# Kernel tuning notes

Hardware: AMD Instinct MI355X
Metric: run time of the kernel (lower is better)

The kernel has to match this reference:

```python
import jax, jax.numpy as jnp
import numpy as np

N_SAMPLES, N_CHANNELS, LOOKBACK, N_ASSETS = 16, 64, 128, 64
HIDDEN = 512
HD = HIDDEN // 2  # per-direction hidden size (bidirectional)


def setup_inputs() -> dict:
    key = jax.random.key(0)
    ks = jax.random.split(key, 9)
    s = 1.0 / np.sqrt(HD)  # PyTorch LSTM init scale
    def u(k, shape):
        return jax.random.uniform(k, shape, jnp.float32, -s, s)
    return {
        "x": jax.random.normal(ks[0], (N_SAMPLES, N_CHANNELS, LOOKBACK, N_ASSETS), jnp.float32),
        "W_ih_f": u(ks[1], (4 * HD, N_CHANNELS)),
        "W_hh_f": u(ks[2], (4 * HD, HD)),
        "b_ih_f": u(ks[3], (4 * HD,)),
        "b_hh_f": u(ks[4], (4 * HD,)),
        "W_ih_b": u(ks[5], (4 * HD, N_CHANNELS)),
        "W_hh_b": u(ks[6], (4 * HD, HD)),
        "b_ih_b": u(ks[7], (4 * HD,)),
        "b_hh_b": u(ks[8], (4 * HD,)),
    }


def _lstm_dir(xp, W_hh, reverse):
    # xp: (T, B, 4*HD) precomputed input projections + biases
    B = xp.shape[1]
    h0 = jnp.zeros((B, HD), xp.dtype)
    c0 = jnp.zeros((B, HD), xp.dtype)

    def step(carry, g_x):
        h, c = carry
        g = g_x + h @ W_hh.T  # (B, 4*HD)
        i, f, gg, o = jnp.split(g, 4, axis=-1)  # PyTorch gate order i,f,g,o
        i = jax.nn.sigmoid(i)
        f = jax.nn.sigmoid(f)
        gg = jnp.tanh(gg)
        o = jax.nn.sigmoid(o)
        c = f * c + i * gg
        h = o * jnp.tanh(c)
        return (h, c), h

    _, hs = jax.lax.scan(step, (h0, c0), xp, reverse=reverse)
    return hs  # (T, B, HD), time-aligned (reverse scan keeps original order)


def reference(x, W_ih_f, W_hh_f, b_ih_f, b_hh_f, W_ih_b, W_hh_b, b_ih_b, b_hh_b):
    S, C, T, A = x.shape
    # (S, C, T, A) -> (T, S*A, C): fuse all samples+assets into one batch
    xs = jnp.transpose(x, (2, 0, 3, 1)).reshape(T, S * A, C)
    xp_f = jnp.einsum('tbc,gc->tbg', xs, W_ih_f) + b_ih_f + b_hh_f
    xp_b = jnp.einsum('tbc,gc->tbg', xs, W_ih_b) + b_ih_b + b_hh_b
    h_f = _lstm_dir(xp_f, W_hh_f, reverse=False)  # (T, S*A, HD)
    h_b = _lstm_dir(xp_b, W_hh_b, reverse=True)   # (T, S*A, HD)
    h = jnp.concatenate([h_f, h_b], axis=-1)      # (T, S*A, HIDDEN)
    # -> (S, HIDDEN, T, A)
    return jnp.transpose(h.reshape(T, S, A, HIDDEN), (1, 3, 0, 2))
```

## Files before the change

kernel.cpp:

```cpp
#include <hip/hip_runtime.h>

#define T_LEN 128
#define WF_OFF 0
#define BI_OFF 1310720
#define XZ_OFF 1441792
#define HZ_OFF 18219008
#define FL_OFF 20316160
#define WS_END 20332544

typedef short bf16x8 __attribute__((ext_vector_type(8)));
typedef float f32x4 __attribute__((ext_vector_type(4)));

#define WAITV0 asm volatile("s_waitcnt vmcnt(0)" ::: "memory")
#define SCHB __builtin_amdgcn_sched_barrier(0)

__device__ __forceinline__ short f32_to_bf16(float f) {
  unsigned u = __float_as_uint(f);
  unsigned r = u + 0x7FFFu + ((u >> 16) & 1u);
  return (short)(r >> 16);
}
__device__ __forceinline__ float sigmoidf_fast(float x) {
  return 1.0f / (1.0f + __expf(-x));
}
__device__ __forceinline__ float tanhf_fast(float x) {
  return 1.0f - 2.0f / (__expf(2.0f * x) + 1.0f);
}

__device__ __forceinline__ void gll16(const void* g, char* lds_generic) {
  __builtin_amdgcn_global_load_lds(
      (const __attribute__((address_space(1))) void*)g,
      (__attribute__((address_space(3))) void*)lds_generic, 16, 0, 0);
}
__device__ __forceinline__ bf16x8 ald16(const void* p) {
  bf16x8 d;
  asm volatile("global_load_dwordx4 %0, %1, off" : "=v"(d) : "v"(p));
  return d;
}
__device__ __forceinline__ f32x4 aldf4(const void* p) {
  f32x4 d;
  asm volatile("global_load_dwordx4 %0, %1, off" : "=v"(d) : "v"(p));
  return d;
}
__device__ __forceinline__ bf16x8 ald16_dev(const void* p) {
  bf16x8 d;
  asm volatile("global_load_dwordx4 %0, %1, off sc0 sc1" : "=v"(d) : "v"(p));
  return d;
}
__device__ __forceinline__ void ast16_dev(void* p, bf16x8 v) {
  asm volatile("global_store_dwordx4 %0, %1, off sc0 sc1" :: "v"(p), "v"(v));
}

__global__ void pack_w(const float* __restrict__ Wih_f, const float* __restrict__ Whh_f,
                       const float* __restrict__ Wih_b, const float* __restrict__ Whh_b,
                       short* __restrict__ wf) {
  int t = blockIdx.x * blockDim.x + threadIdx.x;
  int l = t & 63;
  int r1 = t >> 6;
  int kt = r1 % 10;
  int r2 = r1 / 10;
  int mtl = r2 & 7;
  int r3 = r2 >> 3;
  int m = r3 & 7;
  int dir = r3 >> 3;
  const float* Wih = dir ? Wih_b : Wih_f;
  const float* Whh = dir ? Whh_b : Whh_f;
  int rA = l & 15;
  int row = (rA & 3) * 256 + 32 * m + 4 * mtl + (rA >> 2);
  int kb = kt * 32 + (l >> 4) * 8;
  bf16x8 v;
#pragma unroll
  for (int e = 0; e < 8; ++e) {
    int k = kb + e;
    float f = (k < 64) ? Wih[row * 64 + k] : Whh[row * 256 + (k - 64)];
    v[e] = f32_to_bf16(f);
  }
  long idx = ((((long)dir * 8 + m) * 8 + mtl) * 10 + kt) * 64 + l;
  *reinterpret_cast<bf16x8*>(wf + idx * 8) = v;
}

__global__ void pack_bias(const float* __restrict__ bihf, const float* __restrict__ bhhf,
                          const float* __restrict__ bihb, const float* __restrict__ bhhb,
                          float* __restrict__ bp) {
  int t = blockIdx.x * blockDim.x + threadIdx.x;
  int l = t & 63;
  int mtl = (t >> 6) & 7;
  int m = (t >> 9) & 7;
  int dir = (t >> 12) & 1;
  const float* bih = dir ? bihb : bihf;
  const float* bhh = dir ? bhhb : bhhf;
  int u = 32 * m + 4 * mtl + ((l >> 4) & 3);
  f32x4 v;
#pragma unroll
  for (int r = 0; r < 4; ++r) v[r] = bih[r * 256 + u] + bhh[r * 256 + u];
  long idx = (((long)dir * 8 + m) * 8 + mtl) * 64 + l;
  *reinterpret_cast<f32x4*>(bp + idx * 4) = v;
}

__global__ void pack_x(const float* __restrict__ x, short* __restrict__ xz) {
  int t = blockIdx.x * blockDim.x + threadIdx.x;
  int cs = t & 7;
  int a  = (t >> 3) & 63;
  int tt = (t >> 9) & 127;
  int s  = (t >> 16) & 15;
  bf16x8 v;
#pragma unroll
  for (int e = 0; e < 8; ++e) {
    int c = cs * 8 + e;
    v[e] = f32_to_bf16(x[(((long)s * 64 + c) * 128 + tt) * 64 + a]);
  }
  long idx = (((long)s * 128 + tt) * 64 + a) * 64 + cs * 8;
  *reinterpret_cast<bf16x8*>(xz + idx) = v;
}

__global__ __launch_bounds__(512) void lstm_rec(
    const short* __restrict__ wf, const float* __restrict__ bp,
    const short* __restrict__ xz, short* __restrict__ hz,
    int* __restrict__ flags, float* __restrict__ out) {
  __shared__ __align__(16) char zbuf[40960];
  __shared__ __align__(16) char htr[4096];

  const int bid = blockIdx.x;
  const int m = bid >> 5, g = bid & 31;
  const int dir = g & 1, bb = g >> 1;
  const int tid = threadIdx.x;
  const int w = tid >> 6, l = tid & 63;
  const int lg = l >> 4, ln = l & 15;

  const char* wslice = (const char*)wf +
      ((((long)dir * 8 + m) * 8 + w) * 10) * 1024 + (long)l * 16;
  bf16x8 W0[10];
#pragma unroll
  for (int kt = 0; kt < 10; ++kt) W0[kt] = ald16(wslice + kt * 1024);
  const f32x4 bias4 = aldf4((const char*)bp +
      (((((long)dir * 8 + m) * 8 + w) * 64 + l) * 16));
  WAITV0;

  const char* xzb = (const char*)xz + (long)bb * (128L * 64 * 64 * 2);
  char* const hzg = (char*)hz + (long)g * (2L * 64 * 256 * 2);
  int* const flg = flags + g * T_LEN;

  float cst[4] = {0.f, 0.f, 0.f, 0.f};

  for (int st = 0; st < T_LEN; ++st) {
    const int t = dir ? (T_LEN - 1 - st) : st;

    if (st > 0 && tid == 0) {
      while (__hip_atomic_load(flg + (st - 1), __ATOMIC_RELAXED,
                               __HIP_MEMORY_SCOPE_AGENT) < 8)
        __builtin_amdgcn_s_sleep(2);
    }
    __syncthreads();

    {
      const char* xstep = xzb + (long)t * (64 * 64 * 2);
      {
        const int f = w, kt = f >> 2, nt = f & 3;
        gll16(xstep + (long)(((nt * 16 + ln) * 64 + kt * 32 + lg * 8) * 2),
              zbuf + f * 1024);
      }
      bf16x8 hstg[4];
      if (st == 0) {
#pragma unroll
        for (int j = 0; j < 4; ++j) hstg[j] = (bf16x8)(short)0;
      } else {
        const char* hprev = hzg + (long)((st + 1) & 1) * (64 * 256 * 2);
#pragma unroll
        for (int j = 0; j < 4; ++j) {
          const int f = 8 + 4 * w + j, kt = f >> 2, nt = f & 3;
          hstg[j] = ald16_dev(
              hprev + (long)(((nt * 16 + ln) * 256 + (kt - 2) * 32 + lg * 8) * 2));
        }
      }
      WAITV0; SCHB;
#pragma unroll
      for (int j = 0; j < 4; ++j)
        *reinterpret_cast<bf16x8*>(zbuf + (8 + 4 * w + j) * 1024 + l * 16) = hstg[j];
    }
    __syncthreads();

    f32x4 acc[4];
#pragma unroll
    for (int nt = 0; nt < 4; ++nt) acc[nt] = bias4;
#pragma unroll
    for (int kt = 0; kt < 10; ++kt)
#pragma unroll
      for (int nt = 0; nt < 4; ++nt) {
        bf16x8 b = *reinterpret_cast<const bf16x8*>(
            zbuf + (kt * 4 + nt) * 1024 + l * 16);
        acc[nt] = __builtin_amdgcn_mfma_f32_16x16x32_bf16(W0[kt], b, acc[nt], 0, 0, 0);
      }

    float hv[4];
#pragma unroll
    for (int nt = 0; nt < 4; ++nt) {
      float gi = sigmoidf_fast(acc[nt][0]);
      float gf = sigmoidf_fast(acc[nt][1]);
      float gg = tanhf_fast(acc[nt][2]);
      float go = sigmoidf_fast(acc[nt][3]);
      float cc = gf * cst[nt] + gi * gg;
      cst[nt] = cc;
      hv[nt] = go * tanhf_fast(cc);
    }
#pragma unroll
    for (int nt = 0; nt < 4; ++nt)
      *reinterpret_cast<short*>(htr + (nt * 16 + ln) * 64 + (4 * w + lg) * 2) =
          f32_to_bf16(hv[nt]);

    {
      const long hrow = (long)dir * 256 + 32 * m + 4 * w + lg;
#pragma unroll
      for (int nt = 0; nt < 4; ++nt) {
        const int a = nt * 16 + ln;
        out[(((long)bb * 512 + hrow) * 128 + t) * 64 + a] = hv[nt];
      }
    }
    __syncthreads();

    char* hcur = hzg + (long)(st & 1) * (64 * 256 * 2);
    if (tid < 256) {
      const int a = tid >> 2, seg = tid & 3;
      bf16x8 v = *reinterpret_cast<const bf16x8*>(htr + tid * 16);
      ast16_dev(hcur + (long)((a * 256 + 32 * m + seg * 8) * 2), v);
    }
    WAITV0;
    __syncthreads();
    if (tid == 0)
      __hip_atomic_fetch_add(flg + st, 1, __ATOMIC_RELAXED,
                             __HIP_MEMORY_SCOPE_AGENT);
  }
}

extern "C" void kernel_launch(void* const* d_in, const int* in_sizes, int n_in,
                              void* d_out, int out_size, void* d_ws, size_t ws_size,
                              hipStream_t stream) {
  const float* x     = (const float*)d_in[0];
  const float* Wih_f = (const float*)d_in[1];
  const float* Whh_f = (const float*)d_in[2];
  const float* bih_f = (const float*)d_in[3];
  const float* bhh_f = (const float*)d_in[4];
  const float* Wih_b = (const float*)d_in[5];
  const float* Whh_b = (const float*)d_in[6];
  const float* bih_b = (const float*)d_in[7];
  const float* bhh_b = (const float*)d_in[8];
  float* out = (float*)d_out;

  char* ws = (char*)d_ws;
  short* wf    = (short*)(ws + WF_OFF);
  float* bp    = (float*)(ws + BI_OFF);
  short* xz    = (short*)(ws + XZ_OFF);
  short* hz    = (short*)(ws + HZ_OFF);
  int*   flags = (int*)(ws + FL_OFF);

  hipLaunchKernelGGL(pack_w, dim3(320), dim3(256), 0, stream,
                     Wih_f, Whh_f, Wih_b, Whh_b, wf);
  hipLaunchKernelGGL(pack_bias, dim3(32), dim3(256), 0, stream,
                     bih_f, bhh_f, bih_b, bhh_b, bp);
  hipLaunchKernelGGL(pack_x, dim3(4096), dim3(256), 0, stream, x, xz);
  hipMemsetAsync(ws + FL_OFF, 0, WS_END - FL_OFF, stream);
  hipLaunchKernelGGL(lstm_rec, dim3(256), dim3(512), 0, stream,
                     wf, bp, xz, hz, flags, out);
}
```

Baseline: 627.4 us.

## Interleave forward and backward directions per block to hide inter-block sync latency

Each block now handles both LSTM directions for one sample and hidden slice, using 128 blocks instead of 256. It alternates forward and backward steps, so the cross-block flag wait and hidden-state exchange for one direction overlap with compute for the other. LDS buffers are doubled via dynamic shared memory, and the weights for both directions are held in registers. This halves parallelism and raises register and LDS pressure, in exchange for hiding the per-step global synchronization latency.

Measured after the change: 1.081 ms. +72.3%, slower.

```diff
diff --git a/kernel.cpp b/kernel.cpp
--- a/kernel.cpp
+++ b/kernel.cpp
@@ -7,6 +7,7 @@
 #define HZ_OFF 18219008
 #define FL_OFF 20316160
 #define WS_END 20332544
+#define SMEM_BYTES 90112
 
 typedef short bf16x8 __attribute__((ext_vector_type(8)));
 typedef float f32x4 __attribute__((ext_vector_type(4)));
@@ -116,118 +117,169 @@
     const short* __restrict__ wf, const float* __restrict__ bp,
     const short* __restrict__ xz, short* __restrict__ hz,
     int* __restrict__ flags, float* __restrict__ out) {
-  __shared__ __align__(16) char zbuf[40960];
-  __shared__ __align__(16) char htr[4096];
+  extern __shared__ char smem[];
+  char* const zbA = smem;
+  char* const zbB = smem + 40960;
+  char* const htA = smem + 81920;
+  char* const htB = smem + 86016;
 
   const int bid = blockIdx.x;
-  const int m = bid >> 5, g = bid & 31;
-  const int dir = g & 1, bb = g >> 1;
+  const int m = bid >> 4, s = bid & 15;
   const int tid = threadIdx.x;
   const int w = tid >> 6, l = tid & 63;
   const int lg = l >> 4, ln = l & 15;
 
-  const char* wslice = (const char*)wf +
-      ((((long)dir * 8 + m) * 8 + w) * 10) * 1024 + (long)l * 16;
-  bf16x8 W0[10];
-#pragma unroll
-  for (int kt = 0; kt < 10; ++kt) W0[kt] = ald16(wslice + kt * 1024);
-  const f32x4 bias4 = aldf4((const char*)bp +
-      (((((long)dir * 8 + m) * 8 + w) * 64 + l) * 16));
+  const char* wA = (const char*)wf + (((long)0 * 8 + m) * 8 + w) * 10 * 1024 + (long)l * 16;
+  const char* wB = (const char*)wf + (((long)1 * 8 + m) * 8 + w) * 10 * 1024 + (long)l * 16;
+  bf16x8 WA[10], WB[10];
+#pragma unroll
+  for (int kt = 0; kt < 10; ++kt) {
+    WA[kt] = ald16(wA + kt * 1024);
+    WB[kt] = ald16(wB + kt * 1024);
+  }
+  const f32x4 biasA = aldf4((const char*)bp +
+      ((((long)0 * 8 + m) * 8 + w) * 64 + l) * 16);
+  const f32x4 biasB = aldf4((const char*)bp +
+      ((((long)1 * 8 + m) * 8 + w) * 64 + l) * 16);
   WAITV0;
 
-  const char* xzb = (const char*)xz + (long)bb * (128L * 64 * 64 * 2);
-  char* const hzg = (char*)hz + (long)g * (2L * 64 * 256 * 2);
-  int* const flg = flags + g * T_LEN;
-
-  float cst[4] = {0.f, 0.f, 0.f, 0.f};
+  const char* xzb = (const char*)xz + (long)s * (128L * 64 * 64 * 2);
+  char* const hzA = (char*)hz + (long)(2 * s) * 65536;
+  char* const hzB = (char*)hz + (long)(2 * s + 1) * 65536;
+  int* const flgA = flags + (2 * s) * T_LEN;
+  int* const flgB = flags + (2 * s + 1) * T_LEN;
+
+  float cstA[4] = {0.f, 0.f, 0.f, 0.f};
+  float cstB[4] = {0.f, 0.f, 0.f, 0.f};
+
+  {
+    const char* xstep = xzb;
+    const int kt = w >> 2, nt = w & 3;
+    gll16(xstep + (long)(((nt * 16 + ln) * 64 + kt * 32 + lg * 8) * 2),
+          zbA + w * 1024);
+    bf16x8 z8 = (bf16x8)(short)0;
+#pragma unroll
+    for (int j = 0; j < 4; ++j)
+      *reinterpret_cast<bf16x8*>(zbA + (8 + 4 * w + j) * 1024 + l * 16) = z8;
+  }
+  WAITV0;
+  __syncthreads();
+
+#define COMPUTE(ZB, HT, W_, BIAS, CST, T_, DIRQ) do {                         \
+    f32x4 acc[4];                                                             \
+    _Pragma("unroll")                                                         \
+    for (int nt = 0; nt < 4; ++nt) acc[nt] = (BIAS);                          \
+    _Pragma("unroll")                                                         \
+    for (int kt = 0; kt < 10; ++kt)                                           \
+      _Pragma("unroll")                                                       \
+      for (int nt = 0; nt < 4; ++nt) {                                        \
+        bf16x8 b = *reinterpret_cast<const bf16x8*>(                          \
+            (ZB) + (kt * 4 + nt) * 1024 + l * 16);                            \
+        acc[nt] = __builtin_amdgcn_mfma_f32_16x16x32_bf16(W_[kt], b, acc[nt], 0, 0, 0); \
+      }                                                                       \
+    float hv[4];                                                              \
+    _Pragma("unroll")                                                         \
+    for (int nt = 0; nt < 4; ++nt) {                                          \
+      float gi = sigmoidf_fast(acc[nt][0]);                                   \
+      float gf = sigmoidf_fast(acc[nt][1]);                                   \
+      float gg = tanhf_fast(acc[nt][2]);                                      \
+      float go = sigmoidf_fast(acc[nt][3]);                                   \
+      float cc = gf * (CST)[nt] + gi * gg;                                    \
+      (CST)[nt] = cc;                                                         \
+      hv[nt] = go * tanhf_fast(cc);                                           \
+    }                                                                         \
+    _Pragma("unroll")                                                         \
+    for (int nt = 0; nt < 4; ++nt)                                            \
+      *reinterpret_cast<short*>((HT) + (nt * 16 + ln) * 64 + (4 * w + lg) * 2) = \
+          f32_to_bf16(hv[nt]);                                                \
+    {                                                                         \
+      const long hrow = (long)(DIRQ) * 256 + 32 * m + 4 * w + lg;             \
+      _Pragma("unroll")                                                       \
+      for (int nt = 0; nt < 4; ++nt) {                                        \
+        const int a = nt * 16 + ln;                                           \
+        out[(((long)s * 512 + hrow) * 128 + (T_)) * 64 + a] = hv[nt];         \
+      }                                                                       \
+    }                                                                         \
+  } while (0)
+
+#define PUBLISH(HT, HZ, ST) do {                                              \
+    if (tid < 256) {                                                          \
+      const int a = tid >> 2, seg = tid & 3;                                  \
+      bf16x8 v = *reinterpret_cast<const bf16x8*>((HT) + tid * 16);           \
+      ast16_dev((HZ) + (long)((ST) & 1) * 32768 +                             \
+                (long)((a * 256 + 32 * m + seg * 8) * 2), v);                 \
+    }                                                                         \
+  } while (0)
 
   for (int st = 0; st < T_LEN; ++st) {
-    const int t = dir ? (T_LEN - 1 - st) : st;
-
-    if (st > 0 && tid == 0) {
-      while (__hip_atomic_load(flg + (st - 1), __ATOMIC_RELAXED,
+    const int tA = st, tB = T_LEN - 1 - st;
+
+    COMPUTE(zbA, htA, WA, biasA, cstA, tA, 0);
+    __syncthreads();
+    PUBLISH(htA, hzA, st);
+
+    {
+      const char* xstep = xzb + (long)tB * 8192;
+      const int kt = w >> 2, nt = w & 3;
+      gll16(xstep + (long)(((nt * 16 + ln) * 64 + kt * 32 + lg * 8) * 2),
+            zbB + w * 1024);
+      bf16x8 hstg[4];
+      if (st == 0) {
+#pragma unroll
+        for (int j = 0; j < 4; ++j) hstg[j] = (bf16x8)(short)0;
+      } else {
+        while (__hip_atomic_load(flgB + st - 1, __ATOMIC_RELAXED,
+                                 __HIP_MEMORY_SCOPE_AGENT) < 8)
+          __builtin_amdgcn_s_sleep(2);
+        const char* hprev = hzB + (long)((st + 1) & 1) * 32768;
+#pragma unroll
+        for (int j = 0; j < 4; ++j)
+          hstg[j] = ald16_dev(
+              hprev + (long)(((j * 16 + ln) * 256 + w * 32 + lg * 8) * 2));
+      }
+      WAITV0; SCHB;
+      __syncthreads();
+      if (tid == 0)
+        __hip_atomic_fetch_add(flgA + st, 1, __ATOMIC_RELAXED,
+                               __HIP_MEMORY_SCOPE_AGENT);
+#pragma unroll
+      for (int j = 0; j < 4; ++j)
+        *reinterpret_cast<bf16x8*>(zbB + (8 + 4 * w + j) * 1024 + l * 16) = hstg[j];
+    }
+    __syncthreads();
+
+    COMPUTE(zbB, htB, WB, biasB, cstB, tB, 1);
+    __syncthreads();
+    PUBLISH(htB, hzB, st);
+
+    {
+      const int tA1 = (st < T_LEN - 1) ? st + 1 : st;
+      const char* xstep = xzb + (long)tA1 * 8192;
+      const int kt = w >> 2, nt = w & 3;
+      gll16(xstep + (long)(((nt * 16 + ln) * 64 + kt * 32 + lg * 8) * 2),
+            zbA + w * 1024);
+      while (__hip_atomic_load(flgA + st, __ATOMIC_RELAXED,
                                __HIP_MEMORY_SCOPE_AGENT) < 8)
         __builtin_amdgcn_s_sleep(2);
+      const char* hprev = hzA + (long)(st & 1) * 32768;
+      bf16x8 hstg[4];
+#pragma unroll
+      for (int j = 0; j < 4; ++j)
+        hstg[j] = ald16_dev(
+            hprev + (long)(((j * 16 + ln) * 256 + w * 32 + lg * 8) * 2));
+      WAITV0; SCHB;
+      __syncthreads();
+      if (tid == 0)
+        __hip_atomic_fetch_add(flgB + st, 1, __ATOMIC_RELAXED,
+                               __HIP_MEMORY_SCOPE_AGENT);
+#pragma unroll
+      for (int j = 0; j < 4; ++j)
+        *reinterpret_cast<bf16x8*>(zbA + (8 + 4 * w + j) * 1024 + l * 16) = hstg[j];
     }
     __syncthreads();
-
-    {
-      const char* xstep = xzb + (long)t * (64 * 64 * 2);
-      {
-        const int f = w, kt = f >> 2, nt = f & 3;
-        gll16(xstep + (long)(((nt * 16 + ln) * 64 + kt * 32 + lg * 8) * 2),
-              zbuf + f * 1024);
-      }
-      bf16x8 hstg[4];
-      if (st == 0) {
-#pragma unroll
-        for (int j = 0; j < 4; ++j) hstg[j] = (bf16x8)(short)0;
-      } else {
-        const char* hprev = hzg + (long)((st + 1) & 1) * (64 * 256 * 2);
-#pragma unroll
-        for (int j = 0; j < 4; ++j) {
-          const int f = 8 + 4 * w + j, kt = f >> 2, nt = f & 3;
-          hstg[j] = ald16_dev(
-              hprev + (long)(((nt * 16 + ln) * 256 + (kt - 2) * 32 + lg * 8) * 2));
-        }
-      }
-      WAITV0; SCHB;
-#pragma unroll
-      for (int j = 0; j < 4; ++j)
-        *reinterpret_cast<bf16x8*>(zbuf + (8 + 4 * w + j) * 1024 + l * 16) = hstg[j];
-    }
-    __syncthreads();
-
-    f32x4 acc[4];
-#pragma unroll
-    for (int nt = 0; nt < 4; ++nt) acc[nt] = bias4;
-#pragma unroll
-    for (int kt = 0; kt < 10; ++kt)
-#pragma unroll
-      for (int nt = 0; nt < 4; ++nt) {
-        bf16x8 b = *reinterpret_cast<const bf16x8*>(
-            zbuf + (kt * 4 + nt) * 1024 + l * 16);
-        acc[nt] = __builtin_amdgcn_mfma_f32_16x16x32_bf16(W0[kt], b, acc[nt], 0, 0, 0);
-      }
-
-    float hv[4];
-#pragma unroll
-    for (int nt = 0; nt < 4; ++nt) {
-      float gi = sigmoidf_fast(acc[nt][0]);
-      float gf = sigmoidf_fast(acc[nt][1]);
-      float gg = tanhf_fast(acc[nt][2]);
-      float go = sigmoidf_fast(acc[nt][3]);
-      float cc = gf * cst[nt] + gi * gg;
-      cst[nt] = cc;
-      hv[nt] = go * tanhf_fast(cc);
-    }
-#pragma unroll
-    for (int nt = 0; nt < 4; ++nt)
-      *reinterpret_cast<short*>(htr + (nt * 16 + ln) * 64 + (4 * w + lg) * 2) =
-          f32_to_bf16(hv[nt]);
-
-    {
-      const long hrow = (long)dir * 256 + 32 * m + 4 * w + lg;
-#pragma unroll
-      for (int nt = 0; nt < 4; ++nt) {
-        const int a = nt * 16 + ln;
-        out[(((long)bb * 512 + hrow) * 128 + t) * 64 + a] = hv[nt];
-      }
-    }
-    __syncthreads();
-
-    char* hcur = hzg + (long)(st & 1) * (64 * 256 * 2);
-    if (tid < 256) {
-      const int a = tid >> 2, seg = tid & 3;
-      bf16x8 v = *reinterpret_cast<const bf16x8*>(htr + tid * 16);
-      ast16_dev(hcur + (long)((a * 256 + 32 * m + seg * 8) * 2), v);
-    }
-    WAITV0;
-    __syncthreads();
-    if (tid == 0)
-      __hip_atomic_fetch_add(flg + st, 1, __ATOMIC_RELAXED,
-                             __HIP_MEMORY_SCOPE_AGENT);
-  }
+  }
+#undef COMPUTE
+#undef PUBLISH
 }
 
 extern "C" void kernel_launch(void* const* d_in, const int* in_sizes, int n_in,
@@ -251,12 +303,19 @@
   short* hz    = (short*)(ws + HZ_OFF);
   int*   flags = (int*)(ws + FL_OFF);
 
+  static int smem_set = 0;
+  if (!smem_set) {
+    (void)hipFuncSetAttribute((const void*)lstm_rec,
+                              hipFuncAttributeMaxDynamicSharedMemorySize, SMEM_BYTES);
+    smem_set = 1;
+  }
+
   hipLaunchKernelGGL(pack_w, dim3(320), dim3(256), 0, stream,
                      Wih_f, Whh_f, Wih_b, Whh_b, wf);
   hipLaunchKernelGGL(pack_bias, dim3(32), dim3(256), 0, stream,
                      bih_f, bhh_f, bih_b, bhh_b, bp);
   hipLaunchKernelGGL(pack_x, dim3(4096), dim3(256), 0, stream, x, xz);
   hipMemsetAsync(ws + FL_OFF, 0, WS_END - FL_OFF, stream);
-  hipLaunchKernelGGL(lstm_rec, dim3(256), dim3(512), 0, stream,
+  hipLaunchKernelGGL(lstm_rec, dim3(128), dim3(512), SMEM_BYTES, stream,
                      wf, bp, xz, hz, flags, out);
 }
```

## Split recurrence groups by batch halves to shrink cross-block sync fan-in

Applied to the files above, without the earlier changes.

Re-partitions the LSTM recurrence so each block handles 64 hidden units across two M-tiles per wave for half of the 64-asset batch, which halves the number of blocks that must sync on each step's flag (4 instead of 8). The x-tile prefetch is moved ahead of the flag spin-wait, and the spin-wait is now performed by every thread instead of thread 0 only. The output store is moved after the flag signal so it leaves the critical path. Weights held in registers double per wave, raising register pressure.

Result: faster. 520.0 us (-17.1%).

```diff
diff --git a/kernel.cpp b/kernel.cpp
--- a/kernel.cpp
+++ b/kernel.cpp
@@ -6,7 +6,7 @@
 #define XZ_OFF 1441792
 #define HZ_OFF 18219008
 #define FL_OFF 20316160
-#define WS_END 20332544
+#define WS_END 20348928
 
 typedef short bf16x8 __attribute__((ext_vector_type(8)));
 typedef float f32x4 __attribute__((ext_vector_type(4)));
@@ -58,14 +58,14 @@
   int r1 = t >> 6;
   int kt = r1 % 10;
   int r2 = r1 / 10;
-  int mtl = r2 & 7;
-  int r3 = r2 >> 3;
-  int m = r3 & 7;
-  int dir = r3 >> 3;
+  int mtw = r2 & 15;
+  int r3 = r2 >> 4;
+  int p = r3 & 3;
+  int dir = r3 >> 2;
   const float* Wih = dir ? Wih_b : Wih_f;
   const float* Whh = dir ? Whh_b : Whh_f;
   int rA = l & 15;
-  int row = (rA & 3) * 256 + 32 * m + 4 * mtl + (rA >> 2);
+  int row = (rA & 3) * 256 + 64 * p + 4 * mtw + (rA >> 2);
   int kb = kt * 32 + (l >> 4) * 8;
   bf16x8 v;
 #pragma unroll
@@ -74,7 +74,7 @@
     float f = (k < 64) ? Wih[row * 64 + k] : Whh[row * 256 + (k - 64)];
     v[e] = f32_to_bf16(f);
   }
-  long idx = ((((long)dir * 8 + m) * 8 + mtl) * 10 + kt) * 64 + l;
+  long idx = ((((long)dir * 4 + p) * 16 + mtw) * 10 + kt) * 64 + l;
   *reinterpret_cast<bf16x8*>(wf + idx * 8) = v;
 }
 
@@ -83,16 +83,16 @@
                           float* __restrict__ bp) {
   int t = blockIdx.x * blockDim.x + threadIdx.x;
   int l = t & 63;
-  int mtl = (t >> 6) & 7;
-  int m = (t >> 9) & 7;
+  int mtw = (t >> 6) & 15;
+  int p = (t >> 10) & 3;
   int dir = (t >> 12) & 1;
   const float* bih = dir ? bihb : bihf;
   const float* bhh = dir ? bhhb : bhhf;
-  int u = 32 * m + 4 * mtl + ((l >> 4) & 3);
+  int u = 64 * p + 4 * mtw + ((l >> 4) & 3);
   f32x4 v;
 #pragma unroll
   for (int r = 0; r < 4; ++r) v[r] = bih[r * 256 + u] + bhh[r * 256 + u];
-  long idx = (((long)dir * 8 + m) * 8 + mtl) * 64 + l;
+  long idx = (((long)dir * 4 + p) * 16 + mtw) * 64 + l;
   *reinterpret_cast<f32x4*>(bp + idx * 4) = v;
 }
 
@@ -116,117 +116,138 @@
     const short* __restrict__ wf, const float* __restrict__ bp,
     const short* __restrict__ xz, short* __restrict__ hz,
     int* __restrict__ flags, float* __restrict__ out) {
-  __shared__ __align__(16) char zbuf[40960];
+  __shared__ __align__(16) char zbuf[20480];
   __shared__ __align__(16) char htr[4096];
 
   const int bid = blockIdx.x;
-  const int m = bid >> 5, g = bid & 31;
-  const int dir = g & 1, bb = g >> 1;
+  const int g = bid & 31, r = bid >> 5;
+  const int q = r & 1, p = r >> 1;
+  const int dir = g & 1, s = g >> 1;
   const int tid = threadIdx.x;
   const int w = tid >> 6, l = tid & 63;
   const int lg = l >> 4, ln = l & 15;
 
-  const char* wslice = (const char*)wf +
-      ((((long)dir * 8 + m) * 8 + w) * 10) * 1024 + (long)l * 16;
-  bf16x8 W0[10];
-#pragma unroll
-  for (int kt = 0; kt < 10; ++kt) W0[kt] = ald16(wslice + kt * 1024);
-  const f32x4 bias4 = aldf4((const char*)bp +
-      (((((long)dir * 8 + m) * 8 + w) * 64 + l) * 16));
+  const char* wbase = (const char*)wf +
+      ((((long)dir * 4 + p) * 16 + 2 * w) * 10) * 1024 + (long)l * 16;
+  bf16x8 W[2][10];
+#pragma unroll
+  for (int mtid = 0; mtid < 2; ++mtid)
+#pragma unroll
+    for (int kt = 0; kt < 10; ++kt)
+      W[mtid][kt] = ald16(wbase + (mtid * 10 + kt) * 1024);
+  f32x4 biasv[2];
+#pragma unroll
+  for (int mtid = 0; mtid < 2; ++mtid)
+    biasv[mtid] = aldf4((const char*)bp +
+        (((((long)dir * 4 + p) * 16 + 2 * w + mtid) * 64 + l) * 16));
   WAITV0;
 
-  const char* xzb = (const char*)xz + (long)bb * (128L * 64 * 64 * 2);
-  char* const hzg = (char*)hz + (long)g * (2L * 64 * 256 * 2);
-  int* const flg = flags + g * T_LEN;
-
-  float cst[4] = {0.f, 0.f, 0.f, 0.f};
+  const char* xzb = (const char*)xz + (long)s * (128L * 64 * 64 * 2);
+  char* const hzg = (char*)hz + (long)g * 65536;
+  int* const flg = flags + (g * 2 + q) * T_LEN;
+
+  float cst[2][2] = {{0.f, 0.f}, {0.f, 0.f}};
 
   for (int st = 0; st < T_LEN; ++st) {
     const int t = dir ? (T_LEN - 1 - st) : st;
 
-    if (st > 0 && tid == 0) {
+    {
+      const char* xstep = xzb + (long)t * 8192;
+      if (w < 4) {
+        const int kt = w >> 1, nt = w & 1;
+        gll16(xstep + (long)(((32 * q + nt * 16 + ln) * 64 + kt * 32 + lg * 8) * 2),
+              zbuf + w * 1024);
+      }
+    }
+
+    if (st > 0) {
       while (__hip_atomic_load(flg + (st - 1), __ATOMIC_RELAXED,
-                               __HIP_MEMORY_SCOPE_AGENT) < 8)
+                               __HIP_MEMORY_SCOPE_AGENT) < 4)
         __builtin_amdgcn_s_sleep(2);
     }
+
+    {
+      bf16x8 hstg[2];
+      if (st == 0) {
+#pragma unroll
+        for (int j = 0; j < 2; ++j) hstg[j] = (bf16x8)(short)0;
+      } else {
+        const char* hprev = hzg + (long)((st + 1) & 1) * 32768;
+#pragma unroll
+        for (int j = 0; j < 2; ++j) {
+          const int f = 4 + 2 * w + j, kt = f >> 1, nt = f & 1;
+          hstg[j] = ald16_dev(hprev +
+              (long)(((32 * q + nt * 16 + ln) * 256 + (kt - 2) * 32 + lg * 8) * 2));
+        }
+      }
+      WAITV0; SCHB;
+#pragma unroll
+      for (int j = 0; j < 2; ++j)
+        *reinterpret_cast<bf16x8*>(zbuf + (4 + 2 * w + j) * 1024 + l * 16) = hstg[j];
+    }
     __syncthreads();
 
-    {
-      const char* xstep = xzb + (long)t * (64 * 64 * 2);
-      {
-        const int f = w, kt = f >> 2, nt = f & 3;
-        gll16(xstep + (long)(((nt * 16 + ln) * 64 + kt * 32 + lg * 8) * 2),
-              zbuf + f * 1024);
-      }
-      bf16x8 hstg[4];
-      if (st == 0) {
-#pragma unroll
-        for (int j = 0; j < 4; ++j) hstg[j] = (bf16x8)(short)0;
-      } else {
-        const char* hprev = hzg + (long)((st + 1) & 1) * (64 * 256 * 2);
-#pragma unroll
-        for (int j = 0; j < 4; ++j) {
-          const int f = 8 + 4 * w + j, kt = f >> 2, nt = f & 3;
-          hstg[j] = ald16_dev(
-              hprev + (long)(((nt * 16 + ln) * 256 + (kt - 2) * 32 + lg * 8) * 2));
-        }
-      }
-      WAITV0; SCHB;
-#pragma unroll
-      for (int j = 0; j < 4; ++j)
-        *reinterpret_cast<bf16x8*>(zbuf + (8 + 4 * w + j) * 1024 + l * 16) = hstg[j];
-    }
+    f32x4 acc[2][2];
+#pragma unroll
+    for (int mtid = 0; mtid < 2; ++mtid)
+#pragma unroll
+      for (int nt = 0; nt < 2; ++nt) acc[mtid][nt] = biasv[mtid];
+#pragma unroll
+    for (int kt = 0; kt < 10; ++kt)
+#pragma unroll
+      for (int nt = 0; nt < 2; ++nt) {
+        bf16x8 b = *reinterpret_cast<const bf16x8*>(
+            zbuf + (kt * 2 + nt) * 1024 + l * 16);
+        acc[0][nt] = __builtin_amdgcn_mfma_f32_16x16x32_bf16(W[0][kt], b, acc[0][nt], 0, 0, 0);
+        acc[1][nt] = __builtin_amdgcn_mfma_f32_16x16x32_bf16(W[1][kt], b, acc[1][nt], 0, 0, 0);
+      }
+
+    float hv[2][2];
+#pragma unroll
+    for (int mtid = 0; mtid < 2; ++mtid)
+#pragma unroll
+      for (int nt = 0; nt < 2; ++nt) {
+        float gi = sigmoidf_fast(acc[mtid][nt][0]);
+        float gf = sigmoidf_fast(acc[mtid][nt][1]);
+        float gg = tanhf_fast(acc[mtid][nt][2]);
+        float go = sigmoidf_fast(acc[mtid][nt][3]);
+        float cc = gf * cst[mtid][nt] + gi * gg;
+        cst[mtid][nt] = cc;
+        hv[mtid][nt] = go * tanhf_fast(cc);
+      }
+#pragma unroll
+    for (int mtid = 0; mtid < 2; ++mtid)
+#pragma unroll
+      for (int nt = 0; nt < 2; ++nt)
+        *reinterpret_cast<short*>(htr +
+            ((nt * 16 + ln) * 64 + 8 * w + 4 * mtid + lg) * 2) =
+            f32_to_bf16(hv[mtid][nt]);
     __syncthreads();
 
-    f32x4 acc[4];
-#pragma unroll
-    for (int nt = 0; nt < 4; ++nt) acc[nt] = bias4;
-#pragma unroll
-    for (int kt = 0; kt < 10; ++kt)
-#pragma unroll
-      for (int nt = 0; nt < 4; ++nt) {
-        bf16x8 b = *reinterpret_cast<const bf16x8*>(
-            zbuf + (kt * 4 + nt) * 1024 + l * 16);
-        acc[nt] = __builtin_amdgcn_mfma_f32_16x16x32_bf16(W0[kt], b, acc[nt], 0, 0, 0);
-      }
-
-    float hv[4];
-#pragma unroll
-    for (int nt = 0; nt < 4; ++nt) {
-      float gi = sigmoidf_fast(acc[nt][0]);
-      float gf = sigmoidf_fast(acc[nt][1]);
-      float gg = tanhf_fast(acc[nt][2]);
-      float go = sigmoidf_fast(acc[nt][3]);
-      float cc = gf * cst[nt] + gi * gg;
-      cst[nt] = cc;
-      hv[nt] = go * tanhf_fast(cc);
-    }
-#pragma unroll
-    for (int nt = 0; nt < 4; ++nt)
-      *reinterpret_cast<short*>(htr + (nt * 16 + ln) * 64 + (4 * w + lg) * 2) =
-          f32_to_bf16(hv[nt]);
-
-    {
-      const long hrow = (long)dir * 256 + 32 * m + 4 * w + lg;
-#pragma unroll
-      for (int nt = 0; nt < 4; ++nt) {
-        const int a = nt * 16 + ln;
-        out[(((long)bb * 512 + hrow) * 128 + t) * 64 + a] = hv[nt];
-      }
-    }
-    __syncthreads();
-
-    char* hcur = hzg + (long)(st & 1) * (64 * 256 * 2);
-    if (tid < 256) {
-      const int a = tid >> 2, seg = tid & 3;
-      bf16x8 v = *reinterpret_cast<const bf16x8*>(htr + tid * 16);
-      ast16_dev(hcur + (long)((a * 256 + 32 * m + seg * 8) * 2), v);
+    {
+      char* hcur = hzg + (long)(st & 1) * 32768;
+      if (tid < 256) {
+        const int a_l = tid >> 3, seg = tid & 7;
+        bf16x8 v = *reinterpret_cast<const bf16x8*>(htr + tid * 16);
+        ast16_dev(hcur + (long)(((32 * q + a_l) * 256 + 64 * p + seg * 8) * 2), v);
+      }
     }
     WAITV0;
     __syncthreads();
     if (tid == 0)
       __hip_atomic_fetch_add(flg + st, 1, __ATOMIC_RELAXED,
                              __HIP_MEMORY_SCOPE_AGENT);
+
+    {
+#pragma unroll
+      for (int mtid = 0; mtid < 2; ++mtid)
+#pragma unroll
+        for (int nt = 0; nt < 2; ++nt) {
+          const long u = 64 * p + 8 * w + 4 * mtid + lg;
+          const int a = 32 * q + nt * 16 + ln;
+          out[(((long)s * 512 + dir * 256 + u) * 128 + t) * 64 + a] = hv[mtid][nt];
+        }
+    }
   }
 }
 
```
